# Optimization experiments

Measured on AMD Instinct MI355X. Metric: run time of the kernel, lower is better.

The kernel has to match this reference:

```python
import jax, jax.numpy as jnp
import numpy as np

BATCH, CHANNELS, SEQLEN = 32, 96, 4096
D_INNER, DT_RANK, D_STATE, D_CONV = 256, 16, 16, 4
LN_EPS = 1e-5


def setup_inputs() -> dict:
    key = jax.random.key(0)
    ks = jax.random.split(key, 12)
    d, r, n, k = D_INNER, DT_RANK, D_STATE, D_CONV
    x = jax.random.normal(ks[0], (BATCH, CHANNELS, SEQLEN), jnp.float32)
    in_proj_w = jax.random.normal(ks[1], (2 * d, CHANNELS), jnp.float32) * (1.0 / np.sqrt(CHANNELS))
    in_proj_b = jnp.zeros((2 * d,), jnp.float32)
    conv_w = jax.random.normal(ks[2], (d, 1, k), jnp.float32) * (1.0 / np.sqrt(k))
    conv_b = jnp.zeros((d,), jnp.float32)
    x_proj_w = jax.random.normal(ks[3], (r + 2 * n, d), jnp.float32) * (1.0 / np.sqrt(d))
    dt_proj_w = jax.random.normal(ks[4], (d, r), jnp.float32) * (1.0 / np.sqrt(r))
    dt_proj_b = jax.random.normal(ks[5], (d,), jnp.float32) * 0.1
    out_proj_w = jax.random.normal(ks[6], (d, d), jnp.float32) * (1.0 / np.sqrt(d))
    out_proj_b = jnp.zeros((d,), jnp.float32)
    A_log = jnp.log(jnp.broadcast_to(jnp.arange(1, n + 1, dtype=jnp.float32), (d, n)))
    D_param = jnp.ones((d,), jnp.float32)
    ln1_g = jnp.ones((d,), jnp.float32); ln1_b = jnp.zeros((d,), jnp.float32)
    ln2_g = jnp.ones((d,), jnp.float32); ln2_b = jnp.zeros((d,), jnp.float32)
    return {"x": x, "in_proj_w": in_proj_w, "in_proj_b": in_proj_b,
            "conv_w": conv_w, "conv_b": conv_b, "x_proj_w": x_proj_w,
            "dt_proj_w": dt_proj_w, "dt_proj_b": dt_proj_b,
            "out_proj_w": out_proj_w, "out_proj_b": out_proj_b,
            "A_log": A_log, "D_param": D_param,
            "ln1_g": ln1_g, "ln1_b": ln1_b, "ln2_g": ln2_g, "ln2_b": ln2_b}


def _layernorm(v, g, b):
    m = v.mean(-1, keepdims=True)
    var = v.var(-1, keepdims=True)
    return (v - m) / jnp.sqrt(var + LN_EPS) * g + b


def reference(x, in_proj_w, in_proj_b, conv_w, conv_b, x_proj_w,
              dt_proj_w, dt_proj_b, out_proj_w, out_proj_b,
              A_log, D_param, ln1_g, ln1_b, ln2_g, ln2_b):
    b, c, L = x.shape
    r = dt_proj_w.shape[1]
    n = A_log.shape[1]
    h_in = jnp.transpose(x, (0, 2, 1))            # (b, l, c)
    xz = h_in @ in_proj_w.T + in_proj_b          # (b, l, 2d)
    x_res, z = jnp.split(xz, 2, axis=-1)          # (b, l, d) each
    x_ssm = jnp.transpose(x_res, (0, 2, 1))       # (b, d, l)
    k = conv_w.shape[-1]
    # torch: pad both sides k-1 then slice [:L] == causal left-pad k-1
    x_conv = jax.lax.conv_general_dilated(
        x_ssm, conv_w, (1,), ((k - 1, 0),),
        dimension_numbers=("NCH", "OIH", "NCH"),
        feature_group_count=x_ssm.shape[1]) + conv_b[None, :, None]
    x_conv = jax.nn.silu(x_conv)                  # (b, d, l)
    u = jnp.transpose(x_conv, (0, 2, 1))          # (b, l, d)
    dtbc = u @ x_proj_w.T                         # (b, l, r+2n)
    dt_raw, B_raw, C_raw = jnp.split(dtbc, [r, r + n], axis=-1)
    dt = jax.nn.softplus(dt_raw @ dt_proj_w.T + dt_proj_b)   # (b, l, d)
    A = -jnp.exp(A_log)                           # (d, n)

    def step(hst, inp):
        dt_t, B_t, C_t, u_t = inp                 # (b,d),(b,n),(b,n),(b,d)
        dA = jnp.exp(dt_t[..., None] * A)         # (b, d, n)
        hst = dA * hst + (dt_t * u_t)[..., None] * B_t[:, None, :]
        y_t = jnp.einsum("bdn,bn->bd", hst, C_t)
        return hst, y_t

    xs = (jnp.moveaxis(dt, 1, 0), jnp.moveaxis(B_raw, 1, 0),
          jnp.moveaxis(C_raw, 1, 0), jnp.moveaxis(u, 1, 0))
    h0 = jnp.zeros((b, dt.shape[-1], n), x.dtype)
    _, ys = jax.lax.scan(step, h0, xs)            # ys: (l, b, d)
    y = jnp.moveaxis(ys, 0, 1)                    # (b, l, d)
    y = y + u * D_param
    y = y * jax.nn.silu(z)
    y = _layernorm(y + x_res, ln1_g, ln1_b)
    y_proj = y @ out_proj_w.T + out_proj_b
    y = _layernorm(y + y_proj, ln2_g, ln2_b)      # dropout = identity (eval)
    return y
```

## Files before the change

kernel.cpp:

```cpp
#include <hip/hip_runtime.h>
#include <hip/hip_bf16.h>

typedef unsigned short u16;
typedef __attribute__((ext_vector_type(8))) short short8;
typedef __attribute__((ext_vector_type(4))) float f32x4;
typedef __attribute__((ext_vector_type(2))) float f32x2;

#define BATCH 32
#define CIN   96
#define LSEQ  4096
#define DIN   256
#define NST   16
#define MROWS (BATCH * LSEQ)

__device__ __forceinline__ float b2f(u16 u) {
    union { unsigned int i; float f; } v; v.i = ((unsigned int)u) << 16; return v.f;
}
__device__ __forceinline__ u16 f2b(float f) {
    union { float f; unsigned int i; } v; v.f = f;
    unsigned int i = v.i;
    unsigned int lsb = (i >> 16) & 1u;
    return (u16)((i + 0x7fffu + lsb) >> 16);
}
__device__ __forceinline__ float ldv(const u16* p)   { return b2f(*p); }
__device__ __forceinline__ float ldv(const float* p) { return *p; }
__device__ __forceinline__ void stv(u16* p, float v)   { *p = f2b(v); }
__device__ __forceinline__ void stv(float* p, float v) { *p = v; }

__device__ __forceinline__ void ld8(const u16* p, float* f) {
    short8 v = *(const short8*)p;
    #pragma unroll
    for (int e = 0; e < 8; e++) f[e] = b2f((u16)v[e]);
}
__device__ __forceinline__ void ld8(const float* p, float* f) {
    f32x4 a = *(const f32x4*)p; f32x4 b = *(const f32x4*)(p + 4);
    f[0]=a[0]; f[1]=a[1]; f[2]=a[2]; f[3]=a[3];
    f[4]=b[0]; f[5]=b[1]; f[6]=b[2]; f[7]=b[3];
}

__global__ __launch_bounds__(256) void k0_cvt(
    const float* __restrict__ src, u16* __restrict__ dst, int n)
{
    int i = blockIdx.x * 256 + threadIdx.x;
    if (i < n) dst[i] = f2b(src[i]);
}

__global__ __launch_bounds__(256) void k1_inproj(
    const float* __restrict__ x, const u16* __restrict__ wp,
    const float* __restrict__ bias, u16* __restrict__ xz)
{
    __shared__ u16 AtT[64 * 104];
    int m0 = blockIdx.x * 64;
    int b  = m0 >> 12;
    int l0 = m0 & 4095;
    int n0 = blockIdx.y * 256;
    int t  = threadIdx.x;
    {
        int i = t & 63, c0 = t >> 6;
        for (int c = c0; c < 96; c += 4)
            AtT[i * 104 + c] = f2b(x[((size_t)(b * 96 + c)) * 4096 + l0 + i]);
    }
    __syncthreads();
    int lane = t & 63, wid = t >> 6, q = lane >> 4, ml = lane & 15;
    f32x4 acc[16];
    #pragma unroll
    for (int f = 0; f < 16; f++)
        #pragma unroll
        for (int r = 0; r < 4; r++) acc[f][r] = 0.f;
    int arow = wid * 16 + ml;
    for (int k0 = 0; k0 < 96; k0 += 32) {
        int kb = k0 + q * 8;
        short8 a = *(const short8*)&AtT[arow * 104 + kb];
        #pragma unroll
        for (int f = 0; f < 16; f++) {
            int n = n0 + f * 16 + ml;
            short8 bf = *(const short8*)&wp[(size_t)n * 96 + kb];
            acc[f] = __builtin_amdgcn_mfma_f32_16x16x32_bf16(a, bf, acc[f], 0, 0, 0);
        }
    }
    #pragma unroll
    for (int f = 0; f < 16; f++) {
        int n = n0 + f * 16 + ml;
        float bs = bias[n];
        #pragma unroll
        for (int r = 0; r < 4; r++) {
            int m = m0 + wid * 16 + q * 4 + r;
            xz[(size_t)m * 512 + n] = f2b(acc[f][r] + bs);
        }
    }
}

__global__ __launch_bounds__(256) void k2_conv(
    const u16* __restrict__ xz, const float* __restrict__ cw,
    const float* __restrict__ cb, u16* __restrict__ u)
{
    int d  = threadIdx.x;
    int b  = blockIdx.y;
    int l0 = blockIdx.x * 64;
    float w0 = cw[d * 4 + 0], w1 = cw[d * 4 + 1];
    float w2 = cw[d * 4 + 2], w3 = cw[d * 4 + 3];
    float bias = cb[d];
    size_t rowbase = ((size_t)b * 4096) * 512 + d;
    size_t ubase   = ((size_t)b * 4096) * 256 + d;
    float x0 = (l0 >= 3) ? b2f(xz[rowbase + (size_t)(l0 - 3) * 512]) : 0.f;
    float x1 = (l0 >= 2) ? b2f(xz[rowbase + (size_t)(l0 - 2) * 512]) : 0.f;
    float x2 = (l0 >= 1) ? b2f(xz[rowbase + (size_t)(l0 - 1) * 512]) : 0.f;
    for (int l = l0; l < l0 + 64; l++) {
        float x3 = b2f(xz[rowbase + (size_t)l * 512]);
        float s  = w0 * x0 + w1 * x1 + w2 * x2 + w3 * x3 + bias;
        float sig = 1.f / (1.f + __expf(-s));
        u[ubase + (size_t)l * 256] = f2b(s * sig);
        x0 = x1; x1 = x2; x2 = x3;
    }
}

template<typename DT>
__global__ __launch_bounds__(256) void k3_xproj(
    const u16* __restrict__ u, const u16* __restrict__ xw,
    const float* __restrict__ dw, const float* __restrict__ db,
    DT* __restrict__ dt, float* __restrict__ Bb, float* __restrict__ Cb)
{
    __shared__ float dtbc[64][49];
    int m0 = blockIdx.x * 64;
    int t  = threadIdx.x;
    int lane = t & 63, wid = t >> 6, q = lane >> 4, ml = lane & 15;
    f32x4 acc[3];
    #pragma unroll
    for (int f = 0; f < 3; f++)
        #pragma unroll
        for (int r = 0; r < 4; r++) acc[f][r] = 0.f;
    int arow = wid * 16 + ml;
    const u16* ap = &u[(size_t)(m0 + arow) * 256];
    #pragma unroll
    for (int k0 = 0; k0 < 256; k0 += 32) {
        short8 a = *(const short8*)&ap[k0 + q * 8];
        #pragma unroll
        for (int f = 0; f < 3; f++) {
            short8 bf = *(const short8*)&xw[(size_t)(f * 16 + ml) * 256 + k0 + q * 8];
            acc[f] = __builtin_amdgcn_mfma_f32_16x16x32_bf16(a, bf, acc[f], 0, 0, 0);
        }
    }
    #pragma unroll
    for (int f = 0; f < 3; f++)
        #pragma unroll
        for (int r = 0; r < 4; r++)
            dtbc[wid * 16 + q * 4 + r][f * 16 + ml] = acc[f][r];
    __syncthreads();
    {
        int row = t >> 5, cc = t & 31;
        for (int p = 0; p < 8; p++) {
            int rr = row + p * 8;
            float v = dtbc[rr][16 + cc];
            size_t idx = (size_t)(m0 + rr) * 16 + (cc & 15);
            if (cc < 16) Bb[idx] = v; else Cb[idx] = v;
        }
    }
    {
        int d = t;
        float wr[16];
        #pragma unroll
        for (int j = 0; j < 16; j++) wr[j] = dw[d * 16 + j];
        float bias = db[d];
        for (int r = 0; r < 64; r++) {
            float s = bias;
            #pragma unroll
            for (int j = 0; j < 16; j++) s += dtbc[r][j] * wr[j];
            float sp = (s > 20.f) ? s : __logf(1.f + __expf(s));
            stv(&dt[(size_t)(m0 + r) * 256 + d], sp);
        }
    }
}

template<typename DT>
__global__ __launch_bounds__(256) void k4_scanA(
    const DT* __restrict__ dt, const u16* __restrict__ u,
    const float* __restrict__ Bb, const float* __restrict__ alog,
    float* __restrict__ hloc, float* __restrict__ sdt, int lchunk)
{
    __shared__ float Bs[128 * 16];
    int s = blockIdx.x, b = blockIdx.y;
    int l0 = s * lchunk;
    int d = threadIdx.x;
    float Af[16];
    bool structured = true;
    #pragma unroll
    for (int n = 0; n < 16; n++) {
        Af[n] = -__expf(alog[d * 16 + n]);
        structured = structured && (fabsf(Af[n] + (float)(n + 1)) <= 1e-3f * (n + 1));
    }
    const float* bsrc = &Bb[((size_t)b * 4096 + l0) * 16];
    for (int jj = threadIdx.x; jj < lchunk * 16; jj += 256) Bs[jj] = bsrc[jj];
    __syncthreads();
    size_t base = ((size_t)b * 4096 + l0) * 256 + d;
    size_t o = (((size_t)s * 32 + b) * 256 + d) * 16;
    float sd = 0.f;
    if (structured) {
        f32x2 h2[8];
        #pragma unroll
        for (int k = 0; k < 8; k++) h2[k] = (f32x2){0.f, 0.f};
        for (int i = 0; i < lchunk; i++) {
            float dtv = ldv(&dt[base + (size_t)i * 256]);
            float uv  = b2f(u[base + (size_t)i * 256]);
            sd += dtv;
            float du = dtv * uv;
            float e1 = __expf(-dtv);
            float e1s = e1 * e1;
            f32x2 e2 = (f32x2){e1s, e1s};
            f32x2 p  = (f32x2){e1, e1s};
            f32x2 du2 = (f32x2){du, du};
            const f32x2* B2 = (const f32x2*)&Bs[i * 16];
            #pragma unroll
            for (int k = 0; k < 8; k++) {
                h2[k] = p * h2[k] + du2 * B2[k];
                p = p * e2;
            }
        }
        #pragma unroll
        for (int k = 0; k < 8; k++) *(f32x2*)&hloc[o + 2 * k] = h2[k];
    } else {
        float h[16];
        #pragma unroll
        for (int n = 0; n < 16; n++) h[n] = 0.f;
        for (int i = 0; i < lchunk; i++) {
            float dtv = ldv(&dt[base + (size_t)i * 256]);
            float uv  = b2f(u[base + (size_t)i * 256]);
            sd += dtv;
            float du = dtv * uv;
            #pragma unroll
            for (int n = 0; n < 16; n++) {
                float dA = __expf(dtv * Af[n]);
                h[n] = dA * h[n] + du * Bs[i * 16 + n];
            }
        }
        #pragma unroll
        for (int n = 0; n < 16; n++) hloc[o + n] = h[n];
    }
    sdt[((size_t)s * 32 + b) * 256 + d] = sd;
}

__global__ __launch_bounds__(256) void k5_scanB(
    const float* __restrict__ hloc, const float* __restrict__ sdt,
    const float* __restrict__ alog, float* __restrict__ hin, int nch)
{
    int t = blockIdx.x * 256 + threadIdx.x;
    int b = t >> 12;
    int rem = t & 4095;
    int d = rem >> 4;
    float A = -__expf(alog[rem]);
    float h = 0.f;
    for (int s = 0; s < nch; s++) {
        size_t o = ((size_t)(s * 32 + b)) * 4096 + rem;
        float hl = hloc[o];
        float sd = sdt[((size_t)(s * 32 + b)) * 256 + d];
        hin[o] = h;
        h = __expf(A * sd) * h + hl;
    }
}

template<typename DT, typename TT>
__global__ __launch_bounds__(256) void k6_scanC(
    const DT* __restrict__ dt, const u16* __restrict__ u,
    const float* __restrict__ Bb, const float* __restrict__ Cb,
    const float* __restrict__ alog, const float* __restrict__ hin,
    const u16* __restrict__ xz, const float* __restrict__ Dp,
    TT* __restrict__ tp, int lchunk)
{
    __shared__ float Bs[128 * 16];
    __shared__ float Cs[128 * 16];
    int s = blockIdx.x, b = blockIdx.y;
    int l0 = s * lchunk;
    int d = threadIdx.x;
    float Af[16];
    bool structured = true;
    #pragma unroll
    for (int n = 0; n < 16; n++) {
        Af[n] = -__expf(alog[d * 16 + n]);
        structured = structured && (fabsf(Af[n] + (float)(n + 1)) <= 1e-3f * (n + 1));
    }
    {
        const float* bsrc = &Bb[((size_t)b * 4096 + l0) * 16];
        const float* csrc = &Cb[((size_t)b * 4096 + l0) * 16];
        for (int jj = threadIdx.x; jj < lchunk * 16; jj += 256) {
            Bs[jj] = bsrc[jj]; Cs[jj] = csrc[jj];
        }
    }
    __syncthreads();
    size_t o = (((size_t)s * 32 + b) * 256 + d) * 16;
    float Dv = Dp[d];
    size_t base  = ((size_t)b * 4096 + l0) * 256 + d;
    size_t zbase = ((size_t)b * 4096 + l0) * 512 + d;
    if (structured) {
        f32x2 h2[8];
        #pragma unroll
        for (int k = 0; k < 8; k++) h2[k] = *(const f32x2*)&hin[o + 2 * k];
        for (int i = 0; i < lchunk; i++) {
            float dtv = ldv(&dt[base + (size_t)i * 256]);
            float uv  = b2f(u[base + (size_t)i * 256]);
            float du = dtv * uv;
            float e1 = __expf(-dtv);
            float e1s = e1 * e1;
            f32x2 e2 = (f32x2){e1s, e1s};
            f32x2 p  = (f32x2){e1, e1s};
            f32x2 du2 = (f32x2){du, du};
            f32x2 y2 = (f32x2){0.f, 0.f};
            const f32x2* B2 = (const f32x2*)&Bs[i * 16];
            const f32x2* C2 = (const f32x2*)&Cs[i * 16];
            #pragma unroll
            for (int k = 0; k < 8; k++) {
                h2[k] = p * h2[k] + du2 * B2[k];
                y2 = y2 + h2[k] * C2[k];
                p = p * e2;
            }
            float y = y2[0] + y2[1] + uv * Dv;
            float zv = b2f(xz[zbase + (size_t)i * 512 + 256]);
            float xr = b2f(xz[zbase + (size_t)i * 512]);
            float sig = 1.f / (1.f + __expf(-zv));
            y *= zv * sig;
            stv(&tp[base + (size_t)i * 256], y + xr);
        }
    } else {
        float h[16];
        #pragma unroll
        for (int n = 0; n < 16; n++) h[n] = hin[o + n];
        for (int i = 0; i < lchunk; i++) {
            float dtv = ldv(&dt[base + (size_t)i * 256]);
            float uv  = b2f(u[base + (size_t)i * 256]);
            float du = dtv * uv;
            float y = 0.f;
            #pragma unroll
            for (int n = 0; n < 16; n++) {
                float dA = __expf(dtv * Af[n]);
                h[n] = dA * h[n] + du * Bs[i * 16 + n];
                y += h[n] * Cs[i * 16 + n];
            }
            y += uv * Dv;
            float zv = b2f(xz[zbase + (size_t)i * 512 + 256]);
            float xr = b2f(xz[zbase + (size_t)i * 512]);
            float sig = 1.f / (1.f + __expf(-zv));
            y *= zv * sig;
            stv(&tp[base + (size_t)i * 256], y + xr);
        }
    }
}

template<typename TT>
__global__ __launch_bounds__(256) void k8_final(
    const TT* __restrict__ tb, const u16* __restrict__ ow,
    const float* __restrict__ ob, const float* __restrict__ g1,
    const float* __restrict__ bb1, const float* __restrict__ g2,
    const float* __restrict__ bb2, float* __restrict__ out)
{
    __shared__ u16 Yt[64 * 272];
    int m0 = blockIdx.x * 64;
    int t  = threadIdx.x;
    {
        int r = t >> 2, ccol = (t & 3) * 64;
        const TT* src = &tb[(size_t)(m0 + r) * 256 + ccol];
        u16* dst = &Yt[r * 272 + ccol];
        float sum = 0.f, sq = 0.f;
        for (int jj = 0; jj < 64; jj += 8) {
            float f[8]; ld8(src + jj, f);
            #pragma unroll
            for (int e = 0; e < 8; e++) { sum += f[e]; sq += f[e] * f[e]; }
        }
        sum += __shfl_xor(sum, 1); sq += __shfl_xor(sq, 1);
        sum += __shfl_xor(sum, 2); sq += __shfl_xor(sq, 2);
        float mean = sum * (1.f / 256.f);
        float var  = sq * (1.f / 256.f) - mean * mean;
        float rstd = rsqrtf(var + 1e-5f);
        for (int jj = 0; jj < 64; jj += 8) {
            float f[8]; ld8(src + jj, f);
            #pragma unroll
            for (int e = 0; e < 8; e++) {
                int c = ccol + jj + e;
                dst[jj + e] = f2b((f[e] - mean) * rstd * g1[c] + bb1[c]);
            }
        }
    }
    __syncthreads();
    int lane = t & 63, wid = t >> 6, q = lane >> 4, ml = lane & 15;
    f32x4 acc[16];
    #pragma unroll
    for (int f = 0; f < 16; f++)
        #pragma unroll
        for (int r = 0; r < 4; r++) acc[f][r] = 0.f;
    int arow = wid * 16 + ml;
    #pragma unroll
    for (int k0 = 0; k0 < 256; k0 += 32) {
        short8 a = *(const short8*)&Yt[arow * 272 + k0 + q * 8];
        #pragma unroll
        for (int f = 0; f < 16; f++) {
            short8 bf = *(const short8*)&ow[(size_t)(f * 16 + ml) * 256 + k0 + q * 8];
            acc[f] = __builtin_amdgcn_mfma_f32_16x16x32_bf16(a, bf, acc[f], 0, 0, 0);
        }
    }
    float ps[4] = {0, 0, 0, 0}, psq[4] = {0, 0, 0, 0};
    #pragma unroll
    for (int f = 0; f < 16; f++) {
        int col = f * 16 + ml;
        float obv = ob[col];
        #pragma unroll
        for (int r = 0; r < 4; r++) {
            int row = wid * 16 + q * 4 + r;
            float v = acc[f][r] + obv + b2f(Yt[row * 272 + col]);
            acc[f][r] = v;
            ps[r] += v; psq[r] += v * v;
        }
    }
    #pragma unroll
    for (int msk = 1; msk < 16; msk <<= 1) {
        #pragma unroll
        for (int r = 0; r < 4; r++) {
            ps[r]  += __shfl_xor(ps[r],  msk);
            psq[r] += __shfl_xor(psq[r], msk);
        }
    }
    #pragma unroll
    for (int f = 0; f < 16; f++) {
        int col = f * 16 + ml;
        float g2v = g2[col], b2v = bb2[col];
        #pragma unroll
        for (int r = 0; r < 4; r++) {
            int row = wid * 16 + q * 4 + r;
            float mean = ps[r] * (1.f / 256.f);
            float var  = psq[r] * (1.f / 256.f) - mean * mean;
            float rstd = rsqrtf(var + 1e-5f);
            out[(size_t)(m0 + row) * 256 + col] = (acc[f][r] - mean) * rstd * g2v + b2v;
        }
    }
}

extern "C" void kernel_launch(void* const* d_in, const int* in_sizes, int n_in,
                              void* d_out, int out_size, void* d_ws, size_t ws_size,
                              hipStream_t stream)
{
    const float* x    = (const float*)d_in[0];
    const float* ipw  = (const float*)d_in[1];
    const float* ipb  = (const float*)d_in[2];
    const float* cw   = (const float*)d_in[3];
    const float* cb   = (const float*)d_in[4];
    const float* xpw  = (const float*)d_in[5];
    const float* dpw  = (const float*)d_in[6];
    const float* dpb  = (const float*)d_in[7];
    const float* opw  = (const float*)d_in[8];
    const float* opb  = (const float*)d_in[9];
    const float* alog = (const float*)d_in[10];
    const float* Dp   = (const float*)d_in[11];
    const float* g1   = (const float*)d_in[12];
    const float* b1   = (const float*)d_in[13];
    const float* g2   = (const float*)d_in[14];
    const float* b2   = (const float*)d_in[15];
    float* outp = (float*)d_out;

    char* ws = (char*)d_ws;
    u16*   xz  = (u16*)ws;
    u16*   u   = (u16*)(ws + 134217728);
    float* Bb  = (float*)(ws + 201326592);
    float* Cb  = (float*)(ws + 209715200);
    u16* ipw_b = (u16*)(ws + 218103808);
    u16* xpw_b = ipw_b + 49152;
    u16* opw_b = xpw_b + 12288;
    const size_t base = 218103808 + 262144;

    const size_t T32B = 134217728;
    auto chunkBytes = [](size_t nc) { return nc * (524288 * 2 + 32768); };
    int NC; int DT32; int T32;
    if      (ws_size >= base + 134217728 + chunkBytes(64) + T32B) { NC = 64; DT32 = 1; T32 = 1; }
    else if (ws_size >= base + 134217728 + chunkBytes(64))        { NC = 64; DT32 = 1; T32 = 0; }
    else if (ws_size >= base +  67108864 + chunkBytes(64))        { NC = 64; DT32 = 0; T32 = 0; }
    else                                                          { NC = 32; DT32 = 0; T32 = 0; }
    size_t dtB = DT32 ? 134217728 : 67108864;
    void*  dtp  = (void*)(ws + base);
    float* hloc = (float*)(ws + base + dtB);
    float* hin  = hloc + (size_t)NC * 131072;
    float* sdt  = hin  + (size_t)NC * 131072;
    float* t32  = T32 ? (float*)(ws + base + dtB + chunkBytes((size_t)NC)) : nullptr;
    int lchunk = LSEQ / NC;

    k0_cvt<<<192, 256, 0, stream>>>(ipw, ipw_b, 49152);
    k0_cvt<<<48,  256, 0, stream>>>(xpw, xpw_b, 12288);
    k0_cvt<<<256, 256, 0, stream>>>(opw, opw_b, 65536);
    k1_inproj<<<dim3(2048, 2), 256, 0, stream>>>(x, ipw_b, ipb, xz);
    k2_conv  <<<dim3(64, 32),  256, 0, stream>>>(xz, cw, cb, u);
    if (DT32) {
        float* dt = (float*)dtp;
        k3_xproj<float><<<2048, 256, 0, stream>>>(u, xpw_b, dpw, dpb, dt, Bb, Cb);
        k4_scanA<float><<<dim3(NC, 32), 256, 0, stream>>>(dt, u, Bb, alog, hloc, sdt, lchunk);
        k5_scanB<<<512, 256, 0, stream>>>(hloc, sdt, alog, hin, NC);
        if (T32) {
            k6_scanC<float, float><<<dim3(NC, 32), 256, 0, stream>>>(dt, u, Bb, Cb, alog, hin, xz, Dp, t32, lchunk);
            k8_final<float><<<2048, 256, 0, stream>>>(t32, opw_b, opb, g1, b1, g2, b2, outp);
        } else {
            k6_scanC<float, u16><<<dim3(NC, 32), 256, 0, stream>>>(dt, u, Bb, Cb, alog, hin, xz, Dp, u, lchunk);
            k8_final<u16><<<2048, 256, 0, stream>>>(u, opw_b, opb, g1, b1, g2, b2, outp);
        }
    } else {
        u16* dt = (u16*)dtp;
        k3_xproj<u16><<<2048, 256, 0, stream>>>(u, xpw_b, dpw, dpb, dt, Bb, Cb);
        k4_scanA<u16><<<dim3(NC, 32), 256, 0, stream>>>(dt, u, Bb, alog, hloc, sdt, lchunk);
        k5_scanB<<<512, 256, 0, stream>>>(hloc, sdt, alog, hin, NC);
        k6_scanC<u16, u16><<<dim3(NC, 32), 256, 0, stream>>>(dt, u, Bb, Cb, alog, hin, xz, Dp, u, lchunk);
        k8_final<u16><<<2048, 256, 0, stream>>>(u, opw_b, opb, g1, b1, g2, b2, outp);
    }
}
```

Baseline: 728.0 us.

## Fuse conv into x_proj and scan output pass with out-proj and layernorms

The depthwise conv+SiLU is merged into the x_proj kernel: the block stages u in shared memory and feeds the MFMA from there instead of rereading it from global memory. The final scan pass is merged with gating, residual, both layernorms and the out_proj GEMM, keeping the pre-norm tile in shared memory rather than round-tripping it through a global t32 buffer. The scan state propagation now writes hin in place over hloc, which frees workspace. The fused final kernel needs about 75KB of shared memory and 64 accumulator registers per thread, which may reduce occupancy.

```diff
diff --git a/kernel.cpp b/kernel.cpp
--- a/kernel.cpp
+++ b/kernel.cpp
@@ -90,53 +90,55 @@
     }
 }
 
-__global__ __launch_bounds__(256) void k2_conv(
+template<typename DT>
+__global__ __launch_bounds__(256) void k3_convxproj(
     const u16* __restrict__ xz, const float* __restrict__ cw,
-    const float* __restrict__ cb, u16* __restrict__ u)
-{
-    int d  = threadIdx.x;
-    int b  = blockIdx.y;
-    int l0 = blockIdx.x * 64;
-    float w0 = cw[d * 4 + 0], w1 = cw[d * 4 + 1];
-    float w2 = cw[d * 4 + 2], w3 = cw[d * 4 + 3];
-    float bias = cb[d];
-    size_t rowbase = ((size_t)b * 4096) * 512 + d;
-    size_t ubase   = ((size_t)b * 4096) * 256 + d;
-    float x0 = (l0 >= 3) ? b2f(xz[rowbase + (size_t)(l0 - 3) * 512]) : 0.f;
-    float x1 = (l0 >= 2) ? b2f(xz[rowbase + (size_t)(l0 - 2) * 512]) : 0.f;
-    float x2 = (l0 >= 1) ? b2f(xz[rowbase + (size_t)(l0 - 1) * 512]) : 0.f;
-    for (int l = l0; l < l0 + 64; l++) {
-        float x3 = b2f(xz[rowbase + (size_t)l * 512]);
-        float s  = w0 * x0 + w1 * x1 + w2 * x2 + w3 * x3 + bias;
-        float sig = 1.f / (1.f + __expf(-s));
-        u[ubase + (size_t)l * 256] = f2b(s * sig);
-        x0 = x1; x1 = x2; x2 = x3;
-    }
-}
-
-template<typename DT>
-__global__ __launch_bounds__(256) void k3_xproj(
-    const u16* __restrict__ u, const u16* __restrict__ xw,
+    const float* __restrict__ cb, const u16* __restrict__ xw,
     const float* __restrict__ dw, const float* __restrict__ db,
-    DT* __restrict__ dt, float* __restrict__ Bb, float* __restrict__ Cb)
-{
+    u16* __restrict__ u, DT* __restrict__ dt,
+    float* __restrict__ Bb, float* __restrict__ Cb)
+{
+    __shared__ u16 Us[64 * 264];
     __shared__ float dtbc[64][49];
     int m0 = blockIdx.x * 64;
-    int t  = threadIdx.x;
-    int lane = t & 63, wid = t >> 6, q = lane >> 4, ml = lane & 15;
+    int b  = m0 >> 12;
+    int l0 = m0 & 4095;
+    int d  = threadIdx.x;
+    {
+        float w0 = cw[d * 4 + 0], w1 = cw[d * 4 + 1];
+        float w2 = cw[d * 4 + 2], w3 = cw[d * 4 + 3];
+        float bias = cb[d];
+        size_t rowbase = ((size_t)b * 4096) * 512 + d;
+        size_t ubase   = ((size_t)b * 4096 + l0) * 256 + d;
+        float x0 = (l0 >= 3) ? b2f(xz[rowbase + (size_t)(l0 - 3) * 512]) : 0.f;
+        float x1 = (l0 >= 2) ? b2f(xz[rowbase + (size_t)(l0 - 2) * 512]) : 0.f;
+        float x2 = (l0 >= 1) ? b2f(xz[rowbase + (size_t)(l0 - 1) * 512]) : 0.f;
+        #pragma unroll 8
+        for (int i = 0; i < 64; i++) {
+            float x3 = b2f(xz[rowbase + (size_t)(l0 + i) * 512]);
+            float sv = w0 * x0 + w1 * x1 + w2 * x2 + w3 * x3 + bias;
+            float sig = 1.f / (1.f + __expf(-sv));
+            u16 bv = f2b(sv * sig);
+            Us[i * 264 + d] = bv;
+            u[ubase + (size_t)i * 256] = bv;
+            x0 = x1; x1 = x2; x2 = x3;
+        }
+    }
+    __syncthreads();
+    int lane = d & 63, wid = d >> 6, q = lane >> 4, ml = lane & 15;
     f32x4 acc[3];
     #pragma unroll
     for (int f = 0; f < 3; f++)
         #pragma unroll
         for (int r = 0; r < 4; r++) acc[f][r] = 0.f;
     int arow = wid * 16 + ml;
-    const u16* ap = &u[(size_t)(m0 + arow) * 256];
     #pragma unroll
     for (int k0 = 0; k0 < 256; k0 += 32) {
-        short8 a = *(const short8*)&ap[k0 + q * 8];
+        int kb = k0 + q * 8;
+        short8 a = *(const short8*)&Us[arow * 264 + kb];
         #pragma unroll
         for (int f = 0; f < 3; f++) {
-            short8 bf = *(const short8*)&xw[(size_t)(f * 16 + ml) * 256 + k0 + q * 8];
+            short8 bf = *(const short8*)&xw[(size_t)(f * 16 + ml) * 256 + kb];
             acc[f] = __builtin_amdgcn_mfma_f32_16x16x32_bf16(a, bf, acc[f], 0, 0, 0);
         }
     }
@@ -147,7 +149,7 @@
             dtbc[wid * 16 + q * 4 + r][f * 16 + ml] = acc[f][r];
     __syncthreads();
     {
-        int row = t >> 5, cc = t & 31;
+        int row = d >> 5, cc = d & 31;
         for (int p = 0; p < 8; p++) {
             int rr = row + p * 8;
             float v = dtbc[rr][16 + cc];
@@ -156,7 +158,6 @@
         }
     }
     {
-        int d = t;
         float wr[16];
         #pragma unroll
         for (int j = 0; j < 16; j++) wr[j] = dw[d * 16 + j];
@@ -254,6 +255,185 @@
         float sd = sdt[((size_t)(s * 32 + b)) * 256 + d];
         hin[o] = h;
         h = __expf(A * sd) * h + hl;
+    }
+}
+
+#define TP 260
+template<typename DT>
+__global__ __launch_bounds__(256) void k68_scan_final(
+    const DT* __restrict__ dt, const u16* __restrict__ u,
+    const float* __restrict__ Bb, const float* __restrict__ Cb,
+    const float* __restrict__ alog, const float* __restrict__ hin,
+    const u16* __restrict__ xz, const float* __restrict__ Dp,
+    const u16* __restrict__ ow, const float* __restrict__ ob,
+    const float* __restrict__ g1, const float* __restrict__ bb1,
+    const float* __restrict__ g2, const float* __restrict__ bb2,
+    float* __restrict__ out)
+{
+    __shared__ float t32[64 * TP];
+    __shared__ float Bs[64 * 16];
+    __shared__ float Cs[64 * 16];
+    __shared__ float mrs[64][2];
+    int s = blockIdx.x, b = blockIdx.y;
+    int l0 = s * 64;
+    int d  = threadIdx.x;
+    {
+        const float* bsrc = &Bb[((size_t)b * 4096 + l0) * 16];
+        const float* csrc = &Cb[((size_t)b * 4096 + l0) * 16];
+        for (int jj = d; jj < 64 * 16; jj += 256) { Bs[jj] = bsrc[jj]; Cs[jj] = csrc[jj]; }
+    }
+    __syncthreads();
+    {
+        float Af[16];
+        bool structured = true;
+        #pragma unroll
+        for (int n = 0; n < 16; n++) {
+            Af[n] = -__expf(alog[d * 16 + n]);
+            structured = structured && (fabsf(Af[n] + (float)(n + 1)) <= 1e-3f * (n + 1));
+        }
+        size_t o = (((size_t)s * 32 + b) * 256 + d) * 16;
+        float Dv = Dp[d];
+        size_t base  = ((size_t)b * 4096 + l0) * 256 + d;
+        size_t zbase = ((size_t)b * 4096 + l0) * 512 + d;
+        if (structured) {
+            f32x2 h2[8];
+            #pragma unroll
+            for (int k = 0; k < 8; k++) h2[k] = *(const f32x2*)&hin[o + 2 * k];
+            #pragma unroll 4
+            for (int i = 0; i < 64; i++) {
+                float dtv = ldv(&dt[base + (size_t)i * 256]);
+                float uv  = b2f(u[base + (size_t)i * 256]);
+                float du = dtv * uv;
+                float e1 = __expf(-dtv);
+                float e1s = e1 * e1;
+                f32x2 e2 = (f32x2){e1s, e1s};
+                f32x2 p  = (f32x2){e1, e1s};
+                f32x2 du2 = (f32x2){du, du};
+                f32x2 y2 = (f32x2){0.f, 0.f};
+                const f32x2* B2 = (const f32x2*)&Bs[i * 16];
+                const f32x2* C2 = (const f32x2*)&Cs[i * 16];
+                #pragma unroll
+                for (int k = 0; k < 8; k++) {
+                    h2[k] = p * h2[k] + du2 * B2[k];
+                    y2 = y2 + h2[k] * C2[k];
+                    p = p * e2;
+                }
+                float y = y2[0] + y2[1] + uv * Dv;
+                float zv = b2f(xz[zbase + (size_t)i * 512 + 256]);
+                float xr = b2f(xz[zbase + (size_t)i * 512]);
+                float sig = 1.f / (1.f + __expf(-zv));
+                y *= zv * sig;
+                t32[i * TP + d] = y + xr;
+            }
+        } else {
+            float h[16];
+            #pragma unroll
+            for (int n = 0; n < 16; n++) h[n] = hin[o + n];
+            #pragma unroll 4
+            for (int i = 0; i < 64; i++) {
+                float dtv = ldv(&dt[base + (size_t)i * 256]);
+                float uv  = b2f(u[base + (size_t)i * 256]);
+                float du = dtv * uv;
+                float y = 0.f;
+                #pragma unroll
+                for (int n = 0; n < 16; n++) {
+                    float dA = __expf(dtv * Af[n]);
+                    h[n] = dA * h[n] + du * Bs[i * 16 + n];
+                    y += h[n] * Cs[i * 16 + n];
+                }
+                y += uv * Dv;
+                float zv = b2f(xz[zbase + (size_t)i * 512 + 256]);
+                float xr = b2f(xz[zbase + (size_t)i * 512]);
+                float sig = 1.f / (1.f + __expf(-zv));
+                y *= zv * sig;
+                t32[i * TP + d] = y + xr;
+            }
+        }
+    }
+    __syncthreads();
+    {
+        int r = d >> 2, c0 = (d & 3) * 64;
+        const float* src = &t32[r * TP + c0];
+        float sum = 0.f, sq = 0.f;
+        #pragma unroll
+        for (int jj = 0; jj < 64; jj += 4) {
+            f32x4 v = *(const f32x4*)(src + jj);
+            #pragma unroll
+            for (int e = 0; e < 4; e++) { sum += v[e]; sq += v[e] * v[e]; }
+        }
+        sum += __shfl_xor(sum, 1); sq += __shfl_xor(sq, 1);
+        sum += __shfl_xor(sum, 2); sq += __shfl_xor(sq, 2);
+        float mean = sum * (1.f / 256.f);
+        float var  = sq * (1.f / 256.f) - mean * mean;
+        float rstd = rsqrtf(var + 1e-5f);
+        if ((d & 3) == 0) { mrs[r][0] = mean; mrs[r][1] = rstd; }
+    }
+    __syncthreads();
+    int lane = d & 63, wid = d >> 6, q = lane >> 4, ml = lane & 15;
+    int arow = wid * 16 + ml;
+    float meanA = mrs[arow][0], rstdA = mrs[arow][1];
+    const float* trow = &t32[arow * TP];
+    f32x4 acc[16];
+    #pragma unroll
+    for (int f = 0; f < 16; f++)
+        #pragma unroll
+        for (int r = 0; r < 4; r++) acc[f][r] = 0.f;
+    #pragma unroll
+    for (int k0 = 0; k0 < 256; k0 += 32) {
+        int kb = k0 + q * 8;
+        f32x4 ta = *(const f32x4*)(trow + kb);
+        f32x4 tb = *(const f32x4*)(trow + kb + 4);
+        f32x4 ga = *(const f32x4*)&g1[kb];
+        f32x4 gb = *(const f32x4*)&g1[kb + 4];
+        f32x4 ba = *(const f32x4*)&bb1[kb];
+        f32x4 bbv = *(const f32x4*)&bb1[kb + 4];
+        short8 a;
+        #pragma unroll
+        for (int e = 0; e < 4; e++) {
+            a[e]     = (short)f2b((ta[e] - meanA) * rstdA * ga[e] + ba[e]);
+            a[e + 4] = (short)f2b((tb[e] - meanA) * rstdA * gb[e] + bbv[e]);
+        }
+        #pragma unroll
+        for (int f = 0; f < 16; f++) {
+            short8 bf = *(const short8*)&ow[(size_t)(f * 16 + ml) * 256 + kb];
+            acc[f] = __builtin_amdgcn_mfma_f32_16x16x32_bf16(a, bf, acc[f], 0, 0, 0);
+        }
+    }
+    float ps[4] = {0, 0, 0, 0}, psq[4] = {0, 0, 0, 0};
+    #pragma unroll
+    for (int f = 0; f < 16; f++) {
+        int col = f * 16 + ml;
+        float obv = ob[col];
+        float g1c = g1[col], b1c = bb1[col];
+        #pragma unroll
+        for (int r = 0; r < 4; r++) {
+            int row = wid * 16 + q * 4 + r;
+            float y1 = (t32[row * TP + col] - mrs[row][0]) * mrs[row][1] * g1c + b1c;
+            float v = acc[f][r] + obv + y1;
+            acc[f][r] = v;
+            ps[r] += v; psq[r] += v * v;
+        }
+    }
+    #pragma unroll
+    for (int msk = 1; msk < 16; msk <<= 1) {
+        #pragma unroll
+        for (int r = 0; r < 4; r++) {
+            ps[r]  += __shfl_xor(ps[r],  msk);
+            psq[r] += __shfl_xor(psq[r], msk);
+        }
+    }
+    #pragma unroll
+    for (int f = 0; f < 16; f++) {
+        int col = f * 16 + ml;
+        float g2v = g2[col], b2v = bb2[col];
+        #pragma unroll
+        for (int r = 0; r < 4; r++) {
+            int row = wid * 16 + q * 4 + r;
+            float mean = ps[r] * (1.f / 256.f);
+            float var  = psq[r] * (1.f / 256.f) - mean * mean;
+            float rstd = rsqrtf(var + 1e-5f);
+            out[(size_t)(b * 4096 + l0 + row) * 256 + col] = (acc[f][r] - mean) * rstd * g2v + b2v;
+        }
     }
 }
 
@@ -460,46 +640,41 @@
     u16* ipw_b = (u16*)(ws + 218103808);
     u16* xpw_b = ipw_b + 49152;
     u16* opw_b = xpw_b + 12288;
-    const size_t base = 218103808 + 262144;
-
-    const size_t T32B = 134217728;
-    auto chunkBytes = [](size_t nc) { return nc * (524288 * 2 + 32768); };
-    int NC; int DT32; int T32;
-    if      (ws_size >= base + 134217728 + chunkBytes(64) + T32B) { NC = 64; DT32 = 1; T32 = 1; }
-    else if (ws_size >= base + 134217728 + chunkBytes(64))        { NC = 64; DT32 = 1; T32 = 0; }
-    else if (ws_size >= base +  67108864 + chunkBytes(64))        { NC = 64; DT32 = 0; T32 = 0; }
-    else                                                          { NC = 32; DT32 = 0; T32 = 0; }
-    size_t dtB = DT32 ? 134217728 : 67108864;
-    void*  dtp  = (void*)(ws + base);
-    float* hloc = (float*)(ws + base + dtB);
-    float* hin  = hloc + (size_t)NC * 131072;
-    float* sdt  = hin  + (size_t)NC * 131072;
-    float* t32  = T32 ? (float*)(ws + base + dtB + chunkBytes((size_t)NC)) : nullptr;
-    int lchunk = LSEQ / NC;
+    const size_t wbase = 218103808 + 262144;
 
     k0_cvt<<<192, 256, 0, stream>>>(ipw, ipw_b, 49152);
     k0_cvt<<<48,  256, 0, stream>>>(xpw, xpw_b, 12288);
     k0_cvt<<<256, 256, 0, stream>>>(opw, opw_b, 65536);
     k1_inproj<<<dim3(2048, 2), 256, 0, stream>>>(x, ipw_b, ipb, xz);
-    k2_conv  <<<dim3(64, 32),  256, 0, stream>>>(xz, cw, cb, u);
-    if (DT32) {
-        float* dt = (float*)dtp;
-        k3_xproj<float><<<2048, 256, 0, stream>>>(u, xpw_b, dpw, dpb, dt, Bb, Cb);
-        k4_scanA<float><<<dim3(NC, 32), 256, 0, stream>>>(dt, u, Bb, alog, hloc, sdt, lchunk);
-        k5_scanB<<<512, 256, 0, stream>>>(hloc, sdt, alog, hin, NC);
-        if (T32) {
-            k6_scanC<float, float><<<dim3(NC, 32), 256, 0, stream>>>(dt, u, Bb, Cb, alog, hin, xz, Dp, t32, lchunk);
-            k8_final<float><<<2048, 256, 0, stream>>>(t32, opw_b, opb, g1, b1, g2, b2, outp);
-        } else {
-            k6_scanC<float, u16><<<dim3(NC, 32), 256, 0, stream>>>(dt, u, Bb, Cb, alog, hin, xz, Dp, u, lchunk);
-            k8_final<u16><<<2048, 256, 0, stream>>>(u, opw_b, opb, g1, b1, g2, b2, outp);
-        }
+
+    const size_t scan64 = (size_t)64 * 524288 + (size_t)64 * 32768;
+
+    if (ws_size >= wbase + 134217728 + scan64) {
+        float* dt   = (float*)(ws + wbase);
+        float* hloc = (float*)(ws + wbase + 134217728);
+        float* sdt  = hloc + (size_t)64 * 131072;
+        k3_convxproj<float><<<2048, 256, 0, stream>>>(xz, cw, cb, xpw_b, dpw, dpb, u, dt, Bb, Cb);
+        k4_scanA<float><<<dim3(64, 32), 256, 0, stream>>>(dt, u, Bb, alog, hloc, sdt, 64);
+        k5_scanB<<<512, 256, 0, stream>>>(hloc, sdt, alog, hloc, 64);
+        k68_scan_final<float><<<dim3(64, 32), 256, 0, stream>>>(
+            dt, u, Bb, Cb, alog, hloc, xz, Dp, opw_b, opb, g1, b1, g2, b2, outp);
+    } else if (ws_size >= wbase + 67108864 + scan64) {
+        u16*   dt   = (u16*)(ws + wbase);
+        float* hloc = (float*)(ws + wbase + 67108864);
+        float* sdt  = hloc + (size_t)64 * 131072;
+        k3_convxproj<u16><<<2048, 256, 0, stream>>>(xz, cw, cb, xpw_b, dpw, dpb, u, dt, Bb, Cb);
+        k4_scanA<u16><<<dim3(64, 32), 256, 0, stream>>>(dt, u, Bb, alog, hloc, sdt, 64);
+        k5_scanB<<<512, 256, 0, stream>>>(hloc, sdt, alog, hloc, 64);
+        k68_scan_final<u16><<<dim3(64, 32), 256, 0, stream>>>(
+            dt, u, Bb, Cb, alog, hloc, xz, Dp, opw_b, opb, g1, b1, g2, b2, outp);
     } else {
-        u16* dt = (u16*)dtp;
-        k3_xproj<u16><<<2048, 256, 0, stream>>>(u, xpw_b, dpw, dpb, dt, Bb, Cb);
-        k4_scanA<u16><<<dim3(NC, 32), 256, 0, stream>>>(dt, u, Bb, alog, hloc, sdt, lchunk);
-        k5_scanB<<<512, 256, 0, stream>>>(hloc, sdt, alog, hin, NC);
-        k6_scanC<u16, u16><<<dim3(NC, 32), 256, 0, stream>>>(dt, u, Bb, Cb, alog, hin, xz, Dp, u, lchunk);
+        u16*   dt   = (u16*)(ws + wbase);
+        float* hloc = (float*)(ws + wbase + 67108864);
+        float* sdt  = hloc + (size_t)32 * 131072;
+        k3_convxproj<u16><<<2048, 256, 0, stream>>>(xz, cw, cb, xpw_b, dpw, dpb, u, dt, Bb, Cb);
+        k4_scanA<u16><<<dim3(32, 32), 256, 0, stream>>>(dt, u, Bb, alog, hloc, sdt, 128);
+        k5_scanB<<<512, 256, 0, stream>>>(hloc, sdt, alog, hloc, 32);
+        k6_scanC<u16, u16><<<dim3(32, 32), 256, 0, stream>>>(dt, u, Bb, Cb, alog, hloc, xz, Dp, u, 128);
         k8_final<u16><<<2048, 256, 0, stream>>>(u, opw_b, opb, g1, b1, g2, b2, outp);
     }
 }
```

New measurement: 905.8 us. +24.4%, slower.

## Fuse depthwise conv into x-projection kernel, swizzle final LDS, and drop fp32 intermediate

Applied to the files above, without the earlier changes.

The causal depthwise conv+SiLU is computed inside the x_proj kernel and staged in shared memory, so the MFMA no longer re-reads u from global memory, and one launch is removed. The final kernel's LDS tile now uses an XOR swizzle with 16-byte vector stores instead of padding, and it gets an occupancy hint. The fp32 t32 path is dropped in favour of a bf16 intermediate, which saves workspace and bandwidth but may cost some precision. The scan now reuses hloc in place for hin.

```diff
diff --git a/kernel.cpp b/kernel.cpp
--- a/kernel.cpp
+++ b/kernel.cpp
@@ -90,53 +90,55 @@
     }
 }
 
-__global__ __launch_bounds__(256) void k2_conv(
+template<typename DT>
+__global__ __launch_bounds__(256) void k3_convxproj(
     const u16* __restrict__ xz, const float* __restrict__ cw,
-    const float* __restrict__ cb, u16* __restrict__ u)
-{
-    int d  = threadIdx.x;
-    int b  = blockIdx.y;
-    int l0 = blockIdx.x * 64;
-    float w0 = cw[d * 4 + 0], w1 = cw[d * 4 + 1];
-    float w2 = cw[d * 4 + 2], w3 = cw[d * 4 + 3];
-    float bias = cb[d];
-    size_t rowbase = ((size_t)b * 4096) * 512 + d;
-    size_t ubase   = ((size_t)b * 4096) * 256 + d;
-    float x0 = (l0 >= 3) ? b2f(xz[rowbase + (size_t)(l0 - 3) * 512]) : 0.f;
-    float x1 = (l0 >= 2) ? b2f(xz[rowbase + (size_t)(l0 - 2) * 512]) : 0.f;
-    float x2 = (l0 >= 1) ? b2f(xz[rowbase + (size_t)(l0 - 1) * 512]) : 0.f;
-    for (int l = l0; l < l0 + 64; l++) {
-        float x3 = b2f(xz[rowbase + (size_t)l * 512]);
-        float s  = w0 * x0 + w1 * x1 + w2 * x2 + w3 * x3 + bias;
-        float sig = 1.f / (1.f + __expf(-s));
-        u[ubase + (size_t)l * 256] = f2b(s * sig);
-        x0 = x1; x1 = x2; x2 = x3;
-    }
-}
-
-template<typename DT>
-__global__ __launch_bounds__(256) void k3_xproj(
-    const u16* __restrict__ u, const u16* __restrict__ xw,
+    const float* __restrict__ cb, const u16* __restrict__ xw,
     const float* __restrict__ dw, const float* __restrict__ db,
-    DT* __restrict__ dt, float* __restrict__ Bb, float* __restrict__ Cb)
-{
+    u16* __restrict__ u, DT* __restrict__ dt,
+    float* __restrict__ Bb, float* __restrict__ Cb)
+{
+    __shared__ u16 Us[64 * 264];
     __shared__ float dtbc[64][49];
     int m0 = blockIdx.x * 64;
-    int t  = threadIdx.x;
-    int lane = t & 63, wid = t >> 6, q = lane >> 4, ml = lane & 15;
+    int b  = m0 >> 12;
+    int l0 = m0 & 4095;
+    int d  = threadIdx.x;
+    {
+        float w0 = cw[d * 4 + 0], w1 = cw[d * 4 + 1];
+        float w2 = cw[d * 4 + 2], w3 = cw[d * 4 + 3];
+        float bias = cb[d];
+        size_t rowbase = ((size_t)b * 4096) * 512 + d;
+        size_t ubase   = ((size_t)b * 4096 + l0) * 256 + d;
+        float x0 = (l0 >= 3) ? b2f(xz[rowbase + (size_t)(l0 - 3) * 512]) : 0.f;
+        float x1 = (l0 >= 2) ? b2f(xz[rowbase + (size_t)(l0 - 2) * 512]) : 0.f;
+        float x2 = (l0 >= 1) ? b2f(xz[rowbase + (size_t)(l0 - 1) * 512]) : 0.f;
+        #pragma unroll 8
+        for (int i = 0; i < 64; i++) {
+            float x3 = b2f(xz[rowbase + (size_t)(l0 + i) * 512]);
+            float sv = w0 * x0 + w1 * x1 + w2 * x2 + w3 * x3 + bias;
+            float sig = 1.f / (1.f + __expf(-sv));
+            u16 bv = f2b(sv * sig);
+            Us[i * 264 + d] = bv;
+            u[ubase + (size_t)i * 256] = bv;
+            x0 = x1; x1 = x2; x2 = x3;
+        }
+    }
+    __syncthreads();
+    int lane = d & 63, wid = d >> 6, q = lane >> 4, ml = lane & 15;
     f32x4 acc[3];
     #pragma unroll
     for (int f = 0; f < 3; f++)
         #pragma unroll
         for (int r = 0; r < 4; r++) acc[f][r] = 0.f;
     int arow = wid * 16 + ml;
-    const u16* ap = &u[(size_t)(m0 + arow) * 256];
     #pragma unroll
     for (int k0 = 0; k0 < 256; k0 += 32) {
-        short8 a = *(const short8*)&ap[k0 + q * 8];
+        int kb = k0 + q * 8;
+        short8 a = *(const short8*)&Us[arow * 264 + kb];
         #pragma unroll
         for (int f = 0; f < 3; f++) {
-            short8 bf = *(const short8*)&xw[(size_t)(f * 16 + ml) * 256 + k0 + q * 8];
+            short8 bf = *(const short8*)&xw[(size_t)(f * 16 + ml) * 256 + kb];
             acc[f] = __builtin_amdgcn_mfma_f32_16x16x32_bf16(a, bf, acc[f], 0, 0, 0);
         }
     }
@@ -147,7 +149,7 @@
             dtbc[wid * 16 + q * 4 + r][f * 16 + ml] = acc[f][r];
     __syncthreads();
     {
-        int row = t >> 5, cc = t & 31;
+        int row = d >> 5, cc = d & 31;
         for (int p = 0; p < 8; p++) {
             int rr = row + p * 8;
             float v = dtbc[rr][16 + cc];
@@ -156,7 +158,6 @@
         }
     }
     {
-        int d = t;
         float wr[16];
         #pragma unroll
         for (int j = 0; j < 16; j++) wr[j] = dw[d * 16 + j];
@@ -343,20 +344,21 @@
     }
 }
 
+#define YSWZ(bo, row) ((bo) ^ (((row) & 7) << 4))
 template<typename TT>
-__global__ __launch_bounds__(256) void k8_final(
+__global__ __launch_bounds__(256, 5) void k8_final(
     const TT* __restrict__ tb, const u16* __restrict__ ow,
     const float* __restrict__ ob, const float* __restrict__ g1,
     const float* __restrict__ bb1, const float* __restrict__ g2,
     const float* __restrict__ bb2, float* __restrict__ out)
 {
-    __shared__ u16 Yt[64 * 272];
+    __shared__ u16 Yt[64 * 256];
+    char* Yb = (char*)Yt;
     int m0 = blockIdx.x * 64;
     int t  = threadIdx.x;
     {
         int r = t >> 2, ccol = (t & 3) * 64;
         const TT* src = &tb[(size_t)(m0 + r) * 256 + ccol];
-        u16* dst = &Yt[r * 272 + ccol];
         float sum = 0.f, sq = 0.f;
         for (int jj = 0; jj < 64; jj += 8) {
             float f[8]; ld8(src + jj, f);
@@ -370,11 +372,14 @@
         float rstd = rsqrtf(var + 1e-5f);
         for (int jj = 0; jj < 64; jj += 8) {
             float f[8]; ld8(src + jj, f);
+            short8 v;
             #pragma unroll
             for (int e = 0; e < 8; e++) {
                 int c = ccol + jj + e;
-                dst[jj + e] = f2b((f[e] - mean) * rstd * g1[c] + bb1[c]);
+                v[e] = (short)f2b((f[e] - mean) * rstd * g1[c] + bb1[c]);
             }
+            int bo = r * 512 + (ccol + jj) * 2;
+            *(short8*)(Yb + YSWZ(bo, r)) = v;
         }
     }
     __syncthreads();
@@ -387,7 +392,8 @@
     int arow = wid * 16 + ml;
     #pragma unroll
     for (int k0 = 0; k0 < 256; k0 += 32) {
-        short8 a = *(const short8*)&Yt[arow * 272 + k0 + q * 8];
+        int bo = arow * 512 + (k0 + q * 8) * 2;
+        short8 a = *(const short8*)(Yb + YSWZ(bo, arow));
         #pragma unroll
         for (int f = 0; f < 16; f++) {
             short8 bf = *(const short8*)&ow[(size_t)(f * 16 + ml) * 256 + k0 + q * 8];
@@ -402,7 +408,9 @@
         #pragma unroll
         for (int r = 0; r < 4; r++) {
             int row = wid * 16 + q * 4 + r;
-            float v = acc[f][r] + obv + b2f(Yt[row * 272 + col]);
+            int bo = row * 512 + col * 2;
+            float y1 = b2f(*(const u16*)(Yb + YSWZ(bo, row)));
+            float v = acc[f][r] + obv + y1;
             acc[f][r] = v;
             ps[r] += v; psq[r] += v * v;
         }
@@ -460,46 +468,41 @@
     u16* ipw_b = (u16*)(ws + 218103808);
     u16* xpw_b = ipw_b + 49152;
     u16* opw_b = xpw_b + 12288;
-    const size_t base = 218103808 + 262144;
-
-    const size_t T32B = 134217728;
-    auto chunkBytes = [](size_t nc) { return nc * (524288 * 2 + 32768); };
-    int NC; int DT32; int T32;
-    if      (ws_size >= base + 134217728 + chunkBytes(64) + T32B) { NC = 64; DT32 = 1; T32 = 1; }
-    else if (ws_size >= base + 134217728 + chunkBytes(64))        { NC = 64; DT32 = 1; T32 = 0; }
-    else if (ws_size >= base +  67108864 + chunkBytes(64))        { NC = 64; DT32 = 0; T32 = 0; }
-    else                                                          { NC = 32; DT32 = 0; T32 = 0; }
-    size_t dtB = DT32 ? 134217728 : 67108864;
-    void*  dtp  = (void*)(ws + base);
-    float* hloc = (float*)(ws + base + dtB);
-    float* hin  = hloc + (size_t)NC * 131072;
-    float* sdt  = hin  + (size_t)NC * 131072;
-    float* t32  = T32 ? (float*)(ws + base + dtB + chunkBytes((size_t)NC)) : nullptr;
-    int lchunk = LSEQ / NC;
+    const size_t wbase = 218103808 + 262144;
 
     k0_cvt<<<192, 256, 0, stream>>>(ipw, ipw_b, 49152);
     k0_cvt<<<48,  256, 0, stream>>>(xpw, xpw_b, 12288);
     k0_cvt<<<256, 256, 0, stream>>>(opw, opw_b, 65536);
     k1_inproj<<<dim3(2048, 2), 256, 0, stream>>>(x, ipw_b, ipb, xz);
-    k2_conv  <<<dim3(64, 32),  256, 0, stream>>>(xz, cw, cb, u);
-    if (DT32) {
-        float* dt = (float*)dtp;
-        k3_xproj<float><<<2048, 256, 0, stream>>>(u, xpw_b, dpw, dpb, dt, Bb, Cb);
-        k4_scanA<float><<<dim3(NC, 32), 256, 0, stream>>>(dt, u, Bb, alog, hloc, sdt, lchunk);
-        k5_scanB<<<512, 256, 0, stream>>>(hloc, sdt, alog, hin, NC);
-        if (T32) {
-            k6_scanC<float, float><<<dim3(NC, 32), 256, 0, stream>>>(dt, u, Bb, Cb, alog, hin, xz, Dp, t32, lchunk);
-            k8_final<float><<<2048, 256, 0, stream>>>(t32, opw_b, opb, g1, b1, g2, b2, outp);
-        } else {
-            k6_scanC<float, u16><<<dim3(NC, 32), 256, 0, stream>>>(dt, u, Bb, Cb, alog, hin, xz, Dp, u, lchunk);
-            k8_final<u16><<<2048, 256, 0, stream>>>(u, opw_b, opb, g1, b1, g2, b2, outp);
-        }
+
+    const size_t scan64 = (size_t)64 * 524288 + (size_t)64 * 32768;
+
+    if (ws_size >= wbase + 134217728 + scan64) {
+        float* dt   = (float*)(ws + wbase);
+        float* hloc = (float*)(ws + wbase + 134217728);
+        float* sdt  = hloc + (size_t)64 * 131072;
+        k3_convxproj<float><<<2048, 256, 0, stream>>>(xz, cw, cb, xpw_b, dpw, dpb, u, dt, Bb, Cb);
+        k4_scanA<float><<<dim3(64, 32), 256, 0, stream>>>(dt, u, Bb, alog, hloc, sdt, 64);
+        k5_scanB<<<512, 256, 0, stream>>>(hloc, sdt, alog, hloc, 64);
+        k6_scanC<float, u16><<<dim3(64, 32), 256, 0, stream>>>(dt, u, Bb, Cb, alog, hloc, xz, Dp, u, 64);
+        k8_final<u16><<<2048, 256, 0, stream>>>(u, opw_b, opb, g1, b1, g2, b2, outp);
+    } else if (ws_size >= wbase + 67108864 + scan64) {
+        u16*   dt   = (u16*)(ws + wbase);
+        float* hloc = (float*)(ws + wbase + 67108864);
+        float* sdt  = hloc + (size_t)64 * 131072;
+        k3_convxproj<u16><<<2048, 256, 0, stream>>>(xz, cw, cb, xpw_b, dpw, dpb, u, dt, Bb, Cb);
+        k4_scanA<u16><<<dim3(64, 32), 256, 0, stream>>>(dt, u, Bb, alog, hloc, sdt, 64);
+        k5_scanB<<<512, 256, 0, stream>>>(hloc, sdt, alog, hloc, 64);
+        k6_scanC<u16, u16><<<dim3(64, 32), 256, 0, stream>>>(dt, u, Bb, Cb, alog, hloc, xz, Dp, u, 64);
+        k8_final<u16><<<2048, 256, 0, stream>>>(u, opw_b, opb, g1, b1, g2, b2, outp);
     } else {
-        u16* dt = (u16*)dtp;
-        k3_xproj<u16><<<2048, 256, 0, stream>>>(u, xpw_b, dpw, dpb, dt, Bb, Cb);
-        k4_scanA<u16><<<dim3(NC, 32), 256, 0, stream>>>(dt, u, Bb, alog, hloc, sdt, lchunk);
-        k5_scanB<<<512, 256, 0, stream>>>(hloc, sdt, alog, hin, NC);
-        k6_scanC<u16, u16><<<dim3(NC, 32), 256, 0, stream>>>(dt, u, Bb, Cb, alog, hin, xz, Dp, u, lchunk);
+        u16*   dt   = (u16*)(ws + wbase);
+        float* hloc = (float*)(ws + wbase + 67108864);
+        float* sdt  = hloc + (size_t)32 * 131072;
+        k3_convxproj<u16><<<2048, 256, 0, stream>>>(xz, cw, cb, xpw_b, dpw, dpb, u, dt, Bb, Cb);
+        k4_scanA<u16><<<dim3(32, 32), 256, 0, stream>>>(dt, u, Bb, alog, hloc, sdt, 128);
+        k5_scanB<<<512, 256, 0, stream>>>(hloc, sdt, alog, hloc, 32);
+        k6_scanC<u16, u16><<<dim3(32, 32), 256, 0, stream>>>(dt, u, Bb, Cb, alog, hloc, xz, Dp, u, 128);
         k8_final<u16><<<2048, 256, 0, stream>>>(u, opw_b, opb, g1, b1, g2, b2, outp);
     }
 }
```

Result: slower. 898.0 us (+23.3%).
